# Optimization experiments

Hardware: AMD Instinct MI355X
Metric: run time of the kernel (lower is better)

## Reference

```python
import jax, jax.numpy as jnp
import numpy as np

H, W = 2048, 2048          # frame size (cascade_size)
CS = 227                   # classifier_size
K = 16                     # max components classified per frame (fixed budget)
NC = 4                     # num_classes
THRESH = 0.5               # binarization threshold
MIN_SIZE = 64              # min component pixel count
CC_ITERS = 64              # label-propagation iterations for connected components


def _conv(x, w, stride=1, padding='SAME'):
    return jax.lax.conv_general_dilated(x, w, (stride, stride), padding,
                                        dimension_numbers=('NCHW', 'OIHW', 'NCHW'))


def _cascade(x, w1, w2, w3):
    # stand-in for Unet_plus(1,1): full-res segmentation head -> sigmoid mask
    h = jax.nn.relu(_conv(x, w1))
    h = jax.nn.relu(_conv(h, w2))
    return jax.nn.sigmoid(_conv(h, w3))   # [1,1,H,W]


def _classifier(roi, cw1, cw2, fc):
    # stand-in for CompactNet: roi [B,1,CS,CS] -> logits [B,NC]
    h = jax.nn.relu(_conv(roi, cw1, stride=4, padding='VALID'))
    h = jax.nn.relu(_conv(h, cw2, stride=2, padding='VALID'))
    g = h.mean(axis=(2, 3))               # global average pool -> [B,32]
    return g @ fc


def _connected_components(mask):
    # GPU-style min-index label propagation, 4-connectivity; background label = H*W
    BIG = H * W
    lab = jnp.where(mask, jnp.arange(BIG, dtype=jnp.int32).reshape(H, W), BIG)
    def step(_, lab):
        p = jnp.pad(lab, 1, constant_values=BIG)
        nmin = jnp.minimum(jnp.minimum(p[:-2, 1:-1], p[2:, 1:-1]),
                           jnp.minimum(p[1:-1, :-2], p[1:-1, 2:]))
        return jnp.where(mask, jnp.minimum(lab, nmin), BIG)
    return jax.lax.fori_loop(0, CC_ITERS, step, lab)


def _roi_resize(img, y0, y1, x0, x1):
    # bilinear warp of axis-aligned box [y0:y1, x0:x1] to CS x CS
    t = jnp.linspace(0.0, 1.0, CS)
    gy = y0.astype(jnp.float32) + t * (y1 - y0).astype(jnp.float32)
    gx = x0.astype(jnp.float32) + t * (x1 - x0).astype(jnp.float32)
    yf = jnp.clip(jnp.floor(gy).astype(jnp.int32), 0, H - 2)
    xf = jnp.clip(jnp.floor(gx).astype(jnp.int32), 0, W - 2)
    fy = (gy - yf)[:, None]
    fx = (gx - xf)[None, :]
    v00 = img[yf[:, None], xf[None, :]]
    v01 = img[yf[:, None], (xf + 1)[None, :]]
    v10 = img[(yf + 1)[:, None], xf[None, :]]
    v11 = img[(yf + 1)[:, None], (xf + 1)[None, :]]
    return (1 - fy) * ((1 - fx) * v00 + fx * v01) + fy * ((1 - fx) * v10 + fx * v11)


def _detect(x, w1, w2, w3, cw1, cw2, fc):
    pred_mask = _cascade(x, w1, w2, w3)[0, 0]          # [H,W]
    img = x[0, 0]
    mask = pred_mask > THRESH
    lab = jax.lax.stop_gradient(_connected_components(mask))
    counts = jnp.zeros(H * W + 1, jnp.int32).at[lab.ravel()].add(1)
    counts = counts.at[H * W].set(0)                   # drop background
    cnts, lids = jax.lax.top_k(counts, K)              # K largest components

    def per_comp(lid, cnt):
        cm = lab == lid                                # [H,W] component mask
        valid = (cnt >= MIN_SIZE)
        rowany = cm.any(axis=1)
        colany = cm.any(axis=0)
        y0 = jnp.argmax(rowany); y1 = H - 1 - jnp.argmax(rowany[::-1])
        x0 = jnp.argmax(colany); x1 = W - 1 - jnp.argmax(colany[::-1])
        roi = _roi_resize(img, y0, y1, x0, x1)         # [CS,CS] warped crop
        logits = _classifier(roi[None, None], cw1, cw2, fc)[0]
        return logits, cm, valid

    logits, cms, valids = jax.vmap(per_comp)(lids, cnts)   # [K,NC],[K,H,W],[K]
    return logits, cms, valids


def reference(x, w1, w2, w3, cw1, cw2, fc):
    logits, cms, valids = _detect(x, w1, w2, w3, cw1, cw2, fc)
    onehot = jax.nn.one_hot(jnp.argmax(logits, axis=1), NC) * valids[:, None]
    masks = jnp.einsum('kc,khw->chw', onehot, cms.astype(jnp.float32))
    return jnp.clip(masks, 0.0, 1.0)                   # [NC,H,W] per-class masks


def setup_inputs():
    key = jax.random.key(0)
    ks = jax.random.split(key, 7)
    def nrm(k, shape, fan_in):
        return jax.random.normal(k, shape, jnp.float32) / np.sqrt(fan_in).astype(np.float32)
    return {
        'x':   jax.random.normal(ks[0], (1, 1, H, W), jnp.float32),
        'w1':  nrm(ks[1], (32, 1, 3, 3), 9),
        'w2':  nrm(ks[2], (32, 32, 3, 3), 288),
        'w3':  nrm(ks[3], (1, 32, 1, 1), 32),
        'cw1': nrm(ks[4], (16, 1, 7, 7), 49),
        'cw2': nrm(ks[5], (32, 16, 3, 3), 144),
        'fc':  nrm(ks[6], (32, NC), 32),
    }
```

## Files before the change

### kernel.cpp

```cpp
#include <hip/hip_runtime.h>

#define HH 2048
#define WW 2048
#define HWTOT 4194304
#define BIGL 4194304
#define CSZ 227
#define NCLS 4
#define MINSZ 64
#define TF 1.1920928955078125e-7f
#define EPSB 5e-3f
#define LISTCAP 4000000

#define OFF_LABA 0u
#define OFF_LABB (1u<<24)
#define OFF_H1C  ((1u<<24) + 3538944u)
#define OFF_H2C  ((1u<<24) + 7077888u)
#define OFF_CAND ((1u<<24) + 9437184u)
#define OFF_CAND16 ((1u<<24) + 9437184u + 524288u)
#define OFF_COUNTS (2u<<24)
#define OFF_W2R  ((3u<<24) + 4096u)
#define OFF_W1P  ((3u<<24) + 65536u)
#define OFF_LIST ((3u<<24) + 131072u)

typedef __attribute__((ext_vector_type(8))) short bf16x8;
typedef __attribute__((ext_vector_type(4))) float f32x4;
typedef __attribute__((ext_vector_type(2))) float f32x2;
typedef unsigned int uint;
typedef unsigned short ushort;
typedef unsigned long long u64;

struct Meta {
  int lids[16];
  int valid[16];
  int cls[16];
  int bby0[16], bby1[16], bbx0[16], bbx1[16];
};

__device__ __forceinline__ ushort f2bf(float f) {
  uint u = __float_as_uint(f);
  u += 0x7fffu + ((u >> 16) & 1u);
  return (ushort)(u >> 16);
}
__device__ __forceinline__ float bf2f(ushort h) {
  return __uint_as_float(((uint)h) << 16);
}

#define HSWZ(px, g) ((px) * 32 + ((((g) ^ ((px) & 3) ^ (((px) >> 2) & 3))) << 3))

__global__ __launch_bounds__(256) void prep_kernel(const float* __restrict__ w2,
                                                   const float* __restrict__ w1,
                                                   ushort* __restrict__ wfrag,
                                                   float* __restrict__ w1p) {
  int i = blockIdx.x * 256 + threadIdx.x;
  if (i < 288) {
    int g = i / 72, rem = i - g * 72;
    int t = rem >> 3, r = rem & 7;
    w1p[i] = w1[(g * 8 + r) * 9 + t];
  }
  if (i >= 18432) return;
  int fid = i >> 9, within = i & 511;
  int lane = within >> 3, j = within & 7;
  int tap = fid >> 2, m = (fid >> 1) & 1, p = fid & 1;
  int row = lane & 15, kgrp = lane >> 4;
  int ci = kgrp * 8 + j, oc = m * 16 + row;
  float w = w2[oc * 288 + ci * 9 + tap];
  ushort hb = f2bf(w);
  ushort val = hb;
  if (p) { float lof = w - bf2f(hb); val = f2bf(lof); }
  wfrag[i] = val;
}

__global__ __launch_bounds__(512) void cascade_kernel(
    const float* __restrict__ x, const float* __restrict__ w1p,
    const ushort* __restrict__ wfrag, const float* __restrict__ w3,
    int* __restrict__ lab, int* __restrict__ list, int* __restrict__ list_count) {
  __shared__ float xs[20][36];
  __shared__ __align__(16) short hbuf[2][19584];

  const int tid = threadIdx.x;
  const int ox = blockIdx.x * 32, oy = blockIdx.y * 16;

  for (int i = tid; i < 720; i += 512) {
    int r = i / 36, c = i - r * 36;
    int gy = oy - 2 + r, gx = ox - 2 + c;
    float v = 0.f;
    if ((unsigned)gy < (unsigned)HH && (unsigned)gx < (unsigned)WW) v = x[gy * WW + gx];
    xs[r][c] = v;
  }
  __syncthreads();

  for (int px = tid; px < 612; px += 512) {
    const int hr = px / 34, hc = px - hr * 34;
    const int gy = oy - 1 + hr, gx = ox - 1 + hc;
    const bool inimg = ((unsigned)gy < (unsigned)HH) && ((unsigned)gx < (unsigned)WW);
    float a9[9];
#pragma unroll
    for (int du = 0; du < 3; ++du)
#pragma unroll
      for (int dv = 0; dv < 3; ++dv) a9[du * 3 + dv] = xs[hr + du][hc + dv];
#pragma unroll 1
    for (int g = 0; g < 4; ++g) {
      f32x2 sv2[4];
#pragma unroll
      for (int q = 0; q < 4; ++q) sv2[q] = (f32x2){0.f, 0.f};
#pragma unroll
      for (int t = 0; t < 9; ++t) {
        f32x2 a2 = {a9[t], a9[t]};
        const f32x2* wp = (const f32x2*)&w1p[(g * 9 + t) * 8];
#pragma unroll
        for (int q = 0; q < 4; ++q) {
#if __has_builtin(__builtin_elementwise_fma)
          sv2[q] = __builtin_elementwise_fma(a2, wp[q], sv2[q]);
#else
          sv2[q].x = fmaf(a9[t], wp[q].x, sv2[q].x);
          sv2[q].y = fmaf(a9[t], wp[q].y, sv2[q].y);
#endif
        }
      }
      uint hp[4], lp[4];
#pragma unroll
      for (int q = 0; q < 4; ++q) {
        float s0 = inimg ? fmaxf(sv2[q].x, 0.f) : 0.f;
        float s1 = inimg ? fmaxf(sv2[q].y, 0.f) : 0.f;
        uint h2u;
        asm("v_cvt_pk_bf16_f32 %0, %1, %2" : "=v"(h2u) : "v"(s0), "v"(s1));
        float h0 = __uint_as_float(h2u << 16);
        float h1 = __uint_as_float(h2u & 0xffff0000u);
        uint l2u;
        asm("v_cvt_pk_bf16_f32 %0, %1, %2" : "=v"(l2u) : "v"(s0 - h0), "v"(s1 - h1));
        hp[q] = h2u; lp[q] = l2u;
      }
      *(int4*)&hbuf[0][HSWZ(px, g)] = make_int4(hp[0], hp[1], hp[2], hp[3]);
      *(int4*)&hbuf[1][HSWZ(px, g)] = make_int4(lp[0], lp[1], lp[2], lp[3]);
    }
  }
  __syncthreads();

  const int wv = tid >> 6, lane = tid & 63;
  const int col = lane & 15, kg = lane >> 4;
  const f32x4 zero4 = {0.f, 0.f, 0.f, 0.f};
  f32x4 acc[4][2];
#pragma unroll
  for (int i = 0; i < 4; ++i) { acc[i][0] = zero4; acc[i][1] = zero4; }

  const int4* wf4 = (const int4*)wfrag;
#pragma unroll 3
  for (int tap = 0; tap < 9; ++tap) {
    const int ty = tap / 3, tx = tap - ty * 3;
    bf16x8 a[2][2];
#pragma unroll
    for (int m = 0; m < 2; ++m)
#pragma unroll
      for (int p = 0; p < 2; ++p)
        a[m][p] = __builtin_bit_cast(bf16x8, wf4[(tap * 4 + m * 2 + p) * 64 + lane]);
#pragma unroll
    for (int ni = 0; ni < 4; ++ni) {
      const int nt = wv * 4 + ni;
      const int px = ((nt >> 1) + ty) * 34 + (nt & 1) * 16 + tx + col;
      bf16x8 bh = __builtin_bit_cast(bf16x8, *(const int4*)&hbuf[0][HSWZ(px, kg)]);
      bf16x8 bl = __builtin_bit_cast(bf16x8, *(const int4*)&hbuf[1][HSWZ(px, kg)]);
      acc[ni][0] = __builtin_amdgcn_mfma_f32_16x16x32_bf16(a[0][0], bh, acc[ni][0], 0, 0, 0);
      acc[ni][1] = __builtin_amdgcn_mfma_f32_16x16x32_bf16(a[1][0], bh, acc[ni][1], 0, 0, 0);
      acc[ni][0] = __builtin_amdgcn_mfma_f32_16x16x32_bf16(a[0][1], bh, acc[ni][0], 0, 0, 0);
      acc[ni][1] = __builtin_amdgcn_mfma_f32_16x16x32_bf16(a[1][1], bh, acc[ni][1], 0, 0, 0);
      acc[ni][0] = __builtin_amdgcn_mfma_f32_16x16x32_bf16(a[0][0], bl, acc[ni][0], 0, 0, 0);
      acc[ni][1] = __builtin_amdgcn_mfma_f32_16x16x32_bf16(a[1][0], bl, acc[ni][1], 0, 0, 0);
    }
  }

#pragma unroll 1
  for (int ni = 0; ni < 4; ++ni) {
    const int nt = wv * 4 + ni;
    float z = 0.f;
#pragma unroll
    for (int m = 0; m < 2; ++m)
#pragma unroll
      for (int r = 0; r < 4; ++r)
        z = fmaf(w3[m * 16 + kg * 4 + r], fmaxf(acc[ni][m][r], 0.f), z);
    z += __shfl_xor(z, 16);
    z += __shfl_xor(z, 32);
    const int gy = oy + (nt >> 1), gx = ox + (nt & 1) * 16 + col;
    const int p = gy * WW + gx;
    const bool act = lane < 16;
    if (act) lab[p] = (z > TF) ? p : BIGL;
    bool need = act && (fabsf(z - TF) < EPSB);
    unsigned long long mms = __ballot(need);
    if (mms) {
      int cnt = __popcll(mms);
      int prefix = __popcll(mms & ((1ull << lane) - 1ull));
      int basei = 0;
      if (need && prefix == 0) basei = atomicAdd(list_count, cnt);
      int srcl = __ffsll((long long)mms) - 1;
      basei = __shfl(basei, srcl);
      if (need && basei + prefix < LISTCAP) list[basei + prefix] = p;
    }
  }
}

__global__ __launch_bounds__(256) void recheck_kernel(
    const float* __restrict__ x, const float* __restrict__ w1,
    const float* __restrict__ w2, const float* __restrict__ w3,
    const int* __restrict__ list, const int* __restrict__ list_count,
    int* __restrict__ lab) {
  int n = *list_count;
  if (n > LISTCAP) n = LISTCAP;
  const int half = threadIdx.x & 1;
  for (int i = (blockIdx.x * 256 + threadIdx.x) >> 1; i < n; i += (2048 * 256) >> 1) {
    int p = list[i];
    int py = p >> 11, px = p & 2047;
    float xv[5][5];
#pragma unroll
    for (int u = 0; u < 5; ++u)
#pragma unroll
      for (int v = 0; v < 5; ++v) {
        int gy = py - 2 + u, gx = px - 2 + v;
        xv[u][v] = ((unsigned)gy < (unsigned)HH && (unsigned)gx < (unsigned)WW)
                       ? x[gy * WW + gx] : 0.f;
      }
    double acc2[32];
#pragma unroll
    for (int j = 0; j < 32; ++j) acc2[j] = 0.0;
    const int ci0 = half * 16;
#pragma unroll 1
    for (int ci = ci0; ci < ci0 + 16; ++ci) {
      float h1v[3][3];
#pragma unroll
      for (int u = 0; u < 3; ++u)
#pragma unroll
        for (int v = 0; v < 3; ++v) {
          int gy = py - 1 + u, gx = px - 1 + v;
          float s = 0.f;
#pragma unroll
          for (int t9 = 0; t9 < 9; ++t9)
            s = fmaf(xv[u + t9 / 3][v + t9 % 3], w1[ci * 9 + t9], s);
          bool inb = ((unsigned)gy < (unsigned)HH) && ((unsigned)gx < (unsigned)WW);
          h1v[u][v] = (inb && (s > 0.f)) ? s : 0.f;
        }
#pragma unroll
      for (int dy = 0; dy < 3; ++dy)
#pragma unroll
        for (int dx = 0; dx < 3; ++dx) {
          double hd = (double)h1v[dy][dx];
#pragma unroll
          for (int j = 0; j < 32; ++j)
            acc2[j] = fma(hd, (double)w2[j * 288 + ci * 9 + dy * 3 + dx], acc2[j]);
        }
    }
    double zz = 0.0;
#pragma unroll
    for (int j = 0; j < 32; ++j) {
      double other = __shfl_xor(acc2[j], 1);
      double tot = (half == 0) ? (acc2[j] + other) : (other + acc2[j]);
      zz = fma((double)w3[j], tot > 0.0 ? tot : 0.0, zz);
    }
    if (half == 0) lab[p] = (zz > 1.1920928955078125e-7) ? p : BIGL;
  }
}

__global__ __launch_bounds__(256) void cc16_kernel(const int* __restrict__ in,
                                                   int* __restrict__ out) {
  __shared__ __align__(16) int edgeL[24][100];
  __shared__ __align__(16) int edgeR[24][100];
  __shared__ __align__(16) int4 vtop[8][25];
  __shared__ __align__(16) int4 vbot[8][25];
  const int tid = threadIdx.x;
  const int bx = blockIdx.x & 31, by = blockIdx.x >> 5;
  const int ox0 = bx * 64 - 16, oy0 = by * 64 - 16;
  const bool act = tid < 192;
  const int g = tid % 24, s = tid / 24;
  const int gx = ox0 + g * 4;
  const bool colin = ((unsigned)gx < (unsigned)WW);
  int4 c[12];
#pragma unroll
  for (int r = 0; r < 12; ++r) c[r] = make_int4(BIGL, BIGL, BIGL, BIGL);
  if (act && colin) {
#pragma unroll
    for (int r = 0; r < 12; ++r) {
      int gy = oy0 + s * 12 + r;
      if ((unsigned)gy < (unsigned)HH) c[r] = *(const int4*)(in + gy * WW + gx);
    }
  }
#pragma unroll 1
  for (int step = 0; step < 16; ++step) {
    if (act) {
      *(int4*)&edgeL[g][s * 12 + 0] = make_int4(c[0].x, c[1].x, c[2].x, c[3].x);
      *(int4*)&edgeL[g][s * 12 + 4] = make_int4(c[4].x, c[5].x, c[6].x, c[7].x);
      *(int4*)&edgeL[g][s * 12 + 8] = make_int4(c[8].x, c[9].x, c[10].x, c[11].x);
      *(int4*)&edgeR[g][s * 12 + 0] = make_int4(c[0].w, c[1].w, c[2].w, c[3].w);
      *(int4*)&edgeR[g][s * 12 + 4] = make_int4(c[4].w, c[5].w, c[6].w, c[7].w);
      *(int4*)&edgeR[g][s * 12 + 8] = make_int4(c[8].w, c[9].w, c[10].w, c[11].w);
      vtop[s][g] = c[0];
      vbot[s][g] = c[11];
    }
    __syncthreads();
    if (act) {
      int lf[12], rt[12];
      if (g > 0) {
        int4 a0 = *(const int4*)&edgeR[g - 1][s * 12 + 0];
        int4 a1 = *(const int4*)&edgeR[g - 1][s * 12 + 4];
        int4 a2 = *(const int4*)&edgeR[g - 1][s * 12 + 8];
        lf[0] = a0.x; lf[1] = a0.y; lf[2] = a0.z; lf[3] = a0.w;
        lf[4] = a1.x; lf[5] = a1.y; lf[6] = a1.z; lf[7] = a1.w;
        lf[8] = a2.x; lf[9] = a2.y; lf[10] = a2.z; lf[11] = a2.w;
      } else {
#pragma unroll
        for (int r = 0; r < 12; ++r) lf[r] = BIGL;
      }
      if (g < 23) {
        int4 a0 = *(const int4*)&edgeL[g + 1][s * 12 + 0];
        int4 a1 = *(const int4*)&edgeL[g + 1][s * 12 + 4];
        int4 a2 = *(const int4*)&edgeL[g + 1][s * 12 + 8];
        rt[0] = a0.x; rt[1] = a0.y; rt[2] = a0.z; rt[3] = a0.w;
        rt[4] = a1.x; rt[5] = a1.y; rt[6] = a1.z; rt[7] = a1.w;
        rt[8] = a2.x; rt[9] = a2.y; rt[10] = a2.z; rt[11] = a2.w;
      } else {
#pragma unroll
        for (int r = 0; r < 12; ++r) rt[r] = BIGL;
      }
      int4 prev = (s > 0) ? vbot[s - 1][g] : make_int4(BIGL, BIGL, BIGL, BIGL);
      int4 dnlast = (s < 7) ? vtop[s + 1][g] : make_int4(BIGL, BIGL, BIGL, BIGL);
#pragma unroll
      for (int r = 0; r < 12; ++r) {
        int4 cur = c[r];
        int4 d = (r < 11) ? c[r + 1] : dnlast;
        int4 nr;
        nr.x = (cur.x == BIGL) ? BIGL : min(min(cur.x, cur.y), min(min(prev.x, d.x), lf[r]));
        nr.y = (cur.y == BIGL) ? BIGL : min(min(cur.y, min(cur.x, cur.z)), min(prev.y, d.y));
        nr.z = (cur.z == BIGL) ? BIGL : min(min(cur.z, min(cur.y, cur.w)), min(prev.z, d.z));
        nr.w = (cur.w == BIGL) ? BIGL : min(min(cur.w, min(cur.z, rt[r])), min(prev.w, d.w));
        c[r] = nr;
        prev = cur;
      }
    }
    __syncthreads();
  }
  if (act && g >= 4 && g < 20) {
#pragma unroll
    for (int r = 0; r < 12; ++r) {
      int row = s * 12 + r;
      if (row >= 16 && row < 80) {
        int gy = oy0 + row;
        *(int4*)(out + gy * WW + gx) = c[r];
      }
    }
  }
}

__global__ __launch_bounds__(256) void hist_kernel(const int* __restrict__ lab,
                                                   int* __restrict__ counts) {
  __shared__ int hkey[4096];
  __shared__ int hval[4096];
  int tid = threadIdx.x;
  for (int i = tid; i < 4096; i += 256) { hkey[i] = -1; hval[i] = 0; }
  __syncthreads();
  int t = blockIdx.x * 256 + tid;
  int p = t * 8;
  int4 a = *(const int4*)(lab + p), b = *(const int4*)(lab + p + 4);
  int v[8] = {a.x, a.y, a.z, a.w, b.x, b.y, b.z, b.w};
  int prev = -1, run = 0;
#pragma unroll
  for (int j = 0; j < 8; ++j) {
    int l = v[j];
    if (l == prev) { run++; continue; }
    if (prev >= 0 && prev != BIGL) {
      unsigned hh = (((unsigned)prev * 2654435761u) >> 20) & 4095u;
      for (;;) {
        int k = atomicCAS(&hkey[hh], -1, prev);
        if (k == -1 || k == prev) { atomicAdd(&hval[hh], run); break; }
        hh = (hh + 1) & 4095u;
      }
    }
    prev = l; run = 1;
  }
  if (prev >= 0 && prev != BIGL) {
    unsigned hh = (((unsigned)prev * 2654435761u) >> 20) & 4095u;
    for (;;) {
      int k = atomicCAS(&hkey[hh], -1, prev);
      if (k == -1 || k == prev) { atomicAdd(&hval[hh], run); break; }
      hh = (hh + 1) & 4095u;
    }
  }
  __syncthreads();
  for (int i = tid; i < 4096; i += 256)
    if (hkey[i] >= 0) atomicAdd(&counts[hkey[i]], hval[i]);
}

__global__ __launch_bounds__(256) void cand_kernel(const int* __restrict__ counts,
                                                   int2* __restrict__ cand,
                                                   int* __restrict__ cand_count) {
  int i = blockIdx.x * 256 + threadIdx.x;
  int lane = threadIdx.x & 63;
  int c = (i < HWTOT) ? counts[i] : 0;
  bool hit = (c >= MINSZ);
  unsigned long long m = __ballot(hit);
  if (m) {
    int cnt = __popcll(m);
    int prefix = __popcll(m & ((1ull << lane) - 1ull));
    int base = 0;
    if (hit && prefix == 0) base = atomicAdd(cand_count, cnt);
    int srcl = __ffsll((long long)m) - 1;
    base = __shfl(base, srcl);
    if (hit && base + prefix < 65536) cand[base + prefix] = make_int2(c, i);
  }
}

__global__ __launch_bounds__(256) void top16a_kernel(const int2* __restrict__ cand,
                                                     const int* __restrict__ cand_count,
                                                     u64* __restrict__ cand16) {
  __shared__ u64 skey[256];
  int tid = threadIdx.x;
  int n = *cand_count;
  if (n > 65536) n = 65536;
  u64 prev = ~0ull;
  for (int r = 0; r < 16; ++r) {
    u64 best = 0ull;
    for (int i = blockIdx.x * 256 + tid; i < n; i += 32 * 256) {
      int2 cc = cand[i];
      u64 key = ((u64)(unsigned)cc.x << 32) | (unsigned)(BIGL - cc.y);
      if (key < prev && key > best) best = key;
    }
    skey[tid] = best;
    __syncthreads();
    for (int st = 128; st > 0; st >>= 1) {
      if (tid < st && skey[tid + st] > skey[tid]) skey[tid] = skey[tid + st];
      __syncthreads();
    }
    u64 blockbest = skey[0];
    if (tid == 0) cand16[blockIdx.x * 16 + r] = blockbest;
    prev = blockbest;
    __syncthreads();
  }
}

__global__ __launch_bounds__(256) void top16b_kernel(const u64* __restrict__ cand16,
                                                     Meta* __restrict__ meta) {
  __shared__ u64 skey[256];
  int tid = threadIdx.x;
  u64 k0 = cand16[tid], k1 = cand16[tid + 256];
  u64 prev = ~0ull;
  for (int r = 0; r < 16; ++r) {
    u64 best = 0ull;
    if (k0 < prev && k0 > best) best = k0;
    if (k1 < prev && k1 > best) best = k1;
    skey[tid] = best;
    __syncthreads();
    for (int st = 128; st > 0; st >>= 1) {
      if (tid < st && skey[tid + st] > skey[tid]) skey[tid] = skey[tid + st];
      __syncthreads();
    }
    u64 blockbest = skey[0];
    if (tid == 0) {
      if (blockbest > 0ull) {
        meta->lids[r] = BIGL - (int)(blockbest & 0xffffffffull);
        meta->valid[r] = 1;
      } else {
        meta->lids[r] = -1;
        meta->valid[r] = 0;
      }
    }
    prev = blockbest;
    __syncthreads();
  }
  if (tid < 16) {
    meta->bby0[tid] = HH; meta->bby1[tid] = -1;
    meta->bbx0[tid] = WW; meta->bbx1[tid] = -1;
    meta->cls[tid] = 0;
  }
}

__global__ __launch_bounds__(256) void bbox_kernel(const int* __restrict__ lab,
                                                   Meta* __restrict__ meta) {
  __shared__ int lid_s[16];
  __shared__ int by0[16], by1[16], bx0[16], bx1[16];
  int tid = threadIdx.x;
  if (tid < 16) {
    lid_s[tid] = meta->lids[tid];
    by0[tid] = HH; by1[tid] = -1; bx0[tid] = WW; bx1[tid] = -1;
  }
  __syncthreads();
  int t = blockIdx.x * 256 + tid;
  int p = t * 8;
  int y = p >> 11, xbase = p & 2047;
  int4 a = *(const int4*)(lab + p), b = *(const int4*)(lab + p + 4);
  int v[8] = {a.x, a.y, a.z, a.w, b.x, b.y, b.z, b.w};
  int prev = BIGL, kprev = -1, xs = 0, xe = 0;
#pragma unroll
  for (int j = 0; j < 8; ++j) {
    int l = v[j];
    if (l == prev) { xe = xbase + j; continue; }
    if (kprev >= 0) {
      atomicMin(&by0[kprev], y); atomicMax(&by1[kprev], y);
      atomicMin(&bx0[kprev], xs); atomicMax(&bx1[kprev], xe);
    }
    prev = l; xs = xe = xbase + j; kprev = -1;
    if (l != BIGL) {
      for (int k = 0; k < 16; ++k)
        if (lid_s[k] == l) { kprev = k; break; }
    }
  }
  if (kprev >= 0) {
    atomicMin(&by0[kprev], y); atomicMax(&by1[kprev], y);
    atomicMin(&bx0[kprev], xs); atomicMax(&bx1[kprev], xe);
  }
  __syncthreads();
  if (tid < 16 && by1[tid] >= 0) {
    atomicMin(&meta->bby0[tid], by0[tid]); atomicMax(&meta->bby1[tid], by1[tid]);
    atomicMin(&meta->bbx0[tid], bx0[tid]); atomicMax(&meta->bbx1[tid], bx1[tid]);
  }
}

__global__ __launch_bounds__(256) void cconv1_kernel(const float* __restrict__ img,
                                                     const float* __restrict__ cw1,
                                                     const Meta* __restrict__ meta,
                                                     float* __restrict__ h1c) {
  int k = blockIdx.y, oy = blockIdx.x;
  if (!meta->valid[k]) return;
  __shared__ float srow[7][CSZ];
  float y0 = (float)meta->bby0[k], y1 = (float)meta->bby1[k];
  float x0 = (float)meta->bbx0[k], x1 = (float)meta->bbx1[k];
  for (int idx = threadIdx.x; idx < 7 * CSZ; idx += 256) {
    int rr = idx / CSZ, j = idx - rr * CSZ;
    int i = oy * 4 + rr;
    float ti = (float)i / 226.f, tj = (float)j / 226.f;
    float gy = y0 + ti * (y1 - y0);
    float gx = x0 + tj * (x1 - x0);
    int yf = (int)floorf(gy); yf = yf < 0 ? 0 : (yf > HH - 2 ? HH - 2 : yf);
    int xf = (int)floorf(gx); xf = xf < 0 ? 0 : (xf > WW - 2 ? WW - 2 : xf);
    float fy = gy - (float)yf, fx = gx - (float)xf;
    const float* r0 = img + yf * WW + xf;
    float v00 = r0[0], v01 = r0[1], v10 = r0[WW], v11 = r0[WW + 1];
    srow[rr][j] = (1.f - fy) * ((1.f - fx) * v00 + fx * v01) +
                  fy * ((1.f - fx) * v10 + fx * v11);
  }
  __syncthreads();
  for (int idx = threadIdx.x; idx < 16 * 56; idx += 256) {
    int ch = idx / 56, ox = idx - ch * 56;
    const float* wp = cw1 + ch * 49;
    float s = 0.f;
#pragma unroll
    for (int dy = 0; dy < 7; ++dy)
#pragma unroll
      for (int dx = 0; dx < 7; ++dx)
        s += srow[dy][ox * 4 + dx] * wp[dy * 7 + dx];
    h1c[((k * 16 + ch) * 56 + oy) * 56 + ox] = s > 0.f ? s : 0.f;
  }
}

__global__ __launch_bounds__(256) void cconv2_kernel(const float* __restrict__ h1c,
                                                     const float* __restrict__ cw2,
                                                     const Meta* __restrict__ meta,
                                                     float* __restrict__ h2c) {
  int k = blockIdx.y, oy = blockIdx.x;
  if (!meta->valid[k]) return;
  for (int idx = threadIdx.x; idx < 32 * 27; idx += 256) {
    int ch = idx / 27, ox = idx - ch * 27;
    float s = 0.f;
    for (int ci = 0; ci < 16; ++ci) {
      const float* hp = h1c + ((k * 16 + ci) * 56 + oy * 2) * 56 + ox * 2;
      const float* wp = cw2 + (ch * 16 + ci) * 9;
#pragma unroll
      for (int dy = 0; dy < 3; ++dy)
#pragma unroll
        for (int dx = 0; dx < 3; ++dx) s += hp[dy * 56 + dx] * wp[dy * 3 + dx];
    }
    h2c[((k * 32 + ch) * 27 + oy) * 27 + ox] = s > 0.f ? s : 0.f;
  }
}

__global__ __launch_bounds__(256) void poolfc_kernel(const float* __restrict__ h2c,
                                                     const float* __restrict__ fc,
                                                     Meta* __restrict__ meta) {
  int k = blockIdx.x;
  if (!meta->valid[k]) return;
  __shared__ float sums[8][32];
  int tid = threadIdx.x;
  int c = tid & 31, part = tid >> 5;
  float s = 0.f;
  const float* hp = h2c + (k * 32 + c) * 729;
  for (int j = part; j < 729; j += 8) s += hp[j];
  sums[part][c] = s;
  __syncthreads();
  if (tid < 32) {
    float g = 0.f;
#pragma unroll
    for (int p2 = 0; p2 < 8; ++p2) g += sums[p2][tid];
    sums[0][tid] = g / 729.f;
  }
  __syncthreads();
  if (tid == 0) {
    float best = -1e30f;
    int bi = 0;
    for (int j = 0; j < NCLS; ++j) {
      float lg = 0.f;
      for (int c2 = 0; c2 < 32; ++c2) lg += sums[0][c2] * fc[c2 * NCLS + j];
      if (lg > best) { best = lg; bi = j; }
    }
    meta->cls[k] = bi;
  }
}

__global__ __launch_bounds__(256) void final_kernel(const float* labf,
                                                    const Meta* __restrict__ meta,
                                                    float* out) {
  __shared__ int lid_s[16];
  __shared__ int cls_s[16];
  int tid = threadIdx.x;
  if (tid < 16) {
    lid_s[tid] = meta->valid[tid] ? meta->lids[tid] : -1;
    cls_s[tid] = meta->cls[tid];
  }
  __syncthreads();
  int t = blockIdx.x * 256 + tid;
  int p = t * 4;
  float4 lf = *(const float4*)(labf + p);
  int l4[4] = {__float_as_int(lf.x), __float_as_int(lf.y), __float_as_int(lf.z),
               __float_as_int(lf.w)};
  int cj[4];
#pragma unroll
  for (int j = 0; j < 4; ++j) {
    cj[j] = -1;
    int l = l4[j];
    if (l != BIGL) {
      for (int k = 0; k < 16; ++k)
        if (lid_s[k] == l) { cj[j] = cls_s[k]; break; }
    }
  }
#pragma unroll
  for (int c = 0; c < 4; ++c) {
    float4 w4 = make_float4(cj[0] == c ? 1.f : 0.f, cj[1] == c ? 1.f : 0.f,
                            cj[2] == c ? 1.f : 0.f, cj[3] == c ? 1.f : 0.f);
    *(float4*)(out + (size_t)c * HWTOT + p) = w4;
  }
}

extern "C" void kernel_launch(void* const* d_in, const int* in_sizes, int n_in,
                              void* d_out, int out_size, void* d_ws, size_t ws_size,
                              hipStream_t stream) {
  const float* x = (const float*)d_in[0];
  const float* w1 = (const float*)d_in[1];
  const float* w2 = (const float*)d_in[2];
  const float* w3 = (const float*)d_in[3];
  const float* cw1 = (const float*)d_in[4];
  const float* cw2 = (const float*)d_in[5];
  const float* fc = (const float*)d_in[6];

  char* base = (char*)d_out;
  int* lab_a = (int*)(base + OFF_LABA);
  int* lab_b = (int*)(base + OFF_LABB);
  float* h1c = (float*)(base + OFF_H1C);
  float* h2c = (float*)(base + OFF_H2C);
  int2* cand = (int2*)(base + OFF_CAND);
  u64* cand16 = (u64*)(base + OFF_CAND16);
  int* counts = (int*)(base + OFF_COUNTS);
  ushort* wfrag = (ushort*)(base + OFF_W2R);
  float* w1p = (float*)(base + OFF_W1P);
  int* list = (int*)(base + OFF_LIST);
  int* cand_count = (int*)d_ws;
  int* list_count = (int*)((char*)d_ws + 64);
  Meta* meta = (Meta*)((char*)d_ws + 256);

  hipMemsetAsync(counts, 0, (size_t)(HWTOT + 1) * sizeof(int), stream);
  hipMemsetAsync(d_ws, 0, 128, stream);

  prep_kernel<<<72, 256, 0, stream>>>(w2, w1, wfrag, w1p);
  cascade_kernel<<<dim3(64, 128), 512, 0, stream>>>(x, w1p, wfrag, w3, lab_a, list,
                                                    list_count);
  recheck_kernel<<<2048, 256, 0, stream>>>(x, w1, w2, w3, list, list_count, lab_a);

  for (int l = 0; l < 4; ++l) {
    const int* src = (l & 1) ? lab_b : lab_a;
    int* dst = (l & 1) ? lab_a : lab_b;
    cc16_kernel<<<1024, 256, 0, stream>>>(src, dst);
  }

  hist_kernel<<<2048, 256, 0, stream>>>(lab_a, counts);
  cand_kernel<<<16384, 256, 0, stream>>>(counts, cand, cand_count);
  top16a_kernel<<<32, 256, 0, stream>>>(cand, cand_count, cand16);
  top16b_kernel<<<1, 256, 0, stream>>>(cand16, meta);
  bbox_kernel<<<2048, 256, 0, stream>>>(lab_a, meta);
  cconv1_kernel<<<dim3(56, 16), 256, 0, stream>>>(x, cw1, meta, h1c);
  cconv2_kernel<<<dim3(27, 16), 256, 0, stream>>>(h1c, cw2, meta, h2c);
  poolfc_kernel<<<16, 256, 0, stream>>>(h2c, fc, meta);
  final_kernel<<<4096, 256, 0, stream>>>((const float*)d_out, meta, (float*)d_out);
}
```

Baseline: 661.1 us.

## Fuse label histogram into last CC pass, add early exit, drop workspace memset

```diff
diff --git a/kernel.cpp b/kernel.cpp
--- a/kernel.cpp
+++ b/kernel.cpp
@@ -36,6 +36,13 @@
   int bby0[16], bby1[16], bbx0[16], bbx1[16];
 };
 
+struct CCShared {
+  int edgeL[24][100];
+  int edgeR[24][100];
+  int4 vtop[8][25];
+  int4 vbot[8][25];
+};
+
 __device__ __forceinline__ ushort f2bf(float f) {
   uint u = __float_as_uint(f);
   u += 0x7fffu + ((u >> 16) & 1u);
@@ -50,7 +57,9 @@
 __global__ __launch_bounds__(256) void prep_kernel(const float* __restrict__ w2,
                                                    const float* __restrict__ w1,
                                                    ushort* __restrict__ wfrag,
-                                                   float* __restrict__ w1p) {
+                                                   float* __restrict__ w1p,
+                                                   int* __restrict__ ws) {
+  if (blockIdx.x == 0 && threadIdx.x < 32) ws[threadIdx.x] = 0;
   int i = blockIdx.x * 256 + threadIdx.x;
   if (i < 288) {
     int g = i / 72, rem = i - g * 72;
@@ -257,12 +266,22 @@
   }
 }
 
+__device__ __forceinline__ void hist_add(int* hkey, int* hval, int label, int run) {
+  unsigned hh = (((unsigned)label * 2654435761u) >> 20) & 4095u;
+  for (;;) {
+    int k = atomicCAS(&hkey[hh], -1, label);
+    if (k == -1 || k == label) { atomicAdd(&hval[hh], run); break; }
+    hh = (hh + 1) & 4095u;
+  }
+}
+
 __global__ __launch_bounds__(256) void cc16_kernel(const int* __restrict__ in,
-                                                   int* __restrict__ out) {
-  __shared__ __align__(16) int edgeL[24][100];
-  __shared__ __align__(16) int edgeR[24][100];
-  __shared__ __align__(16) int4 vtop[8][25];
-  __shared__ __align__(16) int4 vbot[8][25];
+                                                   int* __restrict__ out,
+                                                   int* __restrict__ counts,
+                                                   int dohist) {
+  __shared__ __align__(16) char smem[32768];
+  CCShared* S = (CCShared*)smem;
+  __shared__ int chg[2];
   const int tid = threadIdx.x;
   const int bx = blockIdx.x & 31, by = blockIdx.x >> 5;
   const int ox0 = bx * 64 - 16, oy0 = by * 64 - 16;
@@ -280,25 +299,31 @@
       if ((unsigned)gy < (unsigned)HH) c[r] = *(const int4*)(in + gy * WW + gx);
     }
   }
+  if (tid < 2) chg[tid] = 1;
+  __syncthreads();
+
 #pragma unroll 1
   for (int step = 0; step < 16; ++step) {
+    const int cur = step & 1, nxt = cur ^ 1;
     if (act) {
-      *(int4*)&edgeL[g][s * 12 + 0] = make_int4(c[0].x, c[1].x, c[2].x, c[3].x);
-      *(int4*)&edgeL[g][s * 12 + 4] = make_int4(c[4].x, c[5].x, c[6].x, c[7].x);
-      *(int4*)&edgeL[g][s * 12 + 8] = make_int4(c[8].x, c[9].x, c[10].x, c[11].x);
-      *(int4*)&edgeR[g][s * 12 + 0] = make_int4(c[0].w, c[1].w, c[2].w, c[3].w);
-      *(int4*)&edgeR[g][s * 12 + 4] = make_int4(c[4].w, c[5].w, c[6].w, c[7].w);
-      *(int4*)&edgeR[g][s * 12 + 8] = make_int4(c[8].w, c[9].w, c[10].w, c[11].w);
-      vtop[s][g] = c[0];
-      vbot[s][g] = c[11];
-    }
-    __syncthreads();
+      *(int4*)&S->edgeL[g][s * 12 + 0] = make_int4(c[0].x, c[1].x, c[2].x, c[3].x);
+      *(int4*)&S->edgeL[g][s * 12 + 4] = make_int4(c[4].x, c[5].x, c[6].x, c[7].x);
+      *(int4*)&S->edgeL[g][s * 12 + 8] = make_int4(c[8].x, c[9].x, c[10].x, c[11].x);
+      *(int4*)&S->edgeR[g][s * 12 + 0] = make_int4(c[0].w, c[1].w, c[2].w, c[3].w);
+      *(int4*)&S->edgeR[g][s * 12 + 4] = make_int4(c[4].w, c[5].w, c[6].w, c[7].w);
+      *(int4*)&S->edgeR[g][s * 12 + 8] = make_int4(c[8].w, c[9].w, c[10].w, c[11].w);
+      S->vtop[s][g] = c[0];
+      S->vbot[s][g] = c[11];
+    }
+    if (tid == 0) chg[nxt] = 0;
+    __syncthreads();
+    if (chg[cur] == 0) break;
     if (act) {
       int lf[12], rt[12];
       if (g > 0) {
-        int4 a0 = *(const int4*)&edgeR[g - 1][s * 12 + 0];
-        int4 a1 = *(const int4*)&edgeR[g - 1][s * 12 + 4];
-        int4 a2 = *(const int4*)&edgeR[g - 1][s * 12 + 8];
+        int4 a0 = *(const int4*)&S->edgeR[g - 1][s * 12 + 0];
+        int4 a1 = *(const int4*)&S->edgeR[g - 1][s * 12 + 4];
+        int4 a2 = *(const int4*)&S->edgeR[g - 1][s * 12 + 8];
         lf[0] = a0.x; lf[1] = a0.y; lf[2] = a0.z; lf[3] = a0.w;
         lf[4] = a1.x; lf[5] = a1.y; lf[6] = a1.z; lf[7] = a1.w;
         lf[8] = a2.x; lf[9] = a2.y; lf[10] = a2.z; lf[11] = a2.w;
@@ -307,9 +332,9 @@
         for (int r = 0; r < 12; ++r) lf[r] = BIGL;
       }
       if (g < 23) {
-        int4 a0 = *(const int4*)&edgeL[g + 1][s * 12 + 0];
-        int4 a1 = *(const int4*)&edgeL[g + 1][s * 12 + 4];
-        int4 a2 = *(const int4*)&edgeL[g + 1][s * 12 + 8];
+        int4 a0 = *(const int4*)&S->edgeL[g + 1][s * 12 + 0];
+        int4 a1 = *(const int4*)&S->edgeL[g + 1][s * 12 + 4];
+        int4 a2 = *(const int4*)&S->edgeL[g + 1][s * 12 + 8];
         rt[0] = a0.x; rt[1] = a0.y; rt[2] = a0.z; rt[3] = a0.w;
         rt[4] = a1.x; rt[5] = a1.y; rt[6] = a1.z; rt[7] = a1.w;
         rt[8] = a2.x; rt[9] = a2.y; rt[10] = a2.z; rt[11] = a2.w;
@@ -317,23 +342,55 @@
 #pragma unroll
         for (int r = 0; r < 12; ++r) rt[r] = BIGL;
       }
-      int4 prev = (s > 0) ? vbot[s - 1][g] : make_int4(BIGL, BIGL, BIGL, BIGL);
-      int4 dnlast = (s < 7) ? vtop[s + 1][g] : make_int4(BIGL, BIGL, BIGL, BIGL);
+      int4 prev = (s > 0) ? S->vbot[s - 1][g] : make_int4(BIGL, BIGL, BIGL, BIGL);
+      int4 dnlast = (s < 7) ? S->vtop[s + 1][g] : make_int4(BIGL, BIGL, BIGL, BIGL);
+      int diff = 0;
 #pragma unroll
       for (int r = 0; r < 12; ++r) {
-        int4 cur = c[r];
+        int4 cc2 = c[r];
         int4 d = (r < 11) ? c[r + 1] : dnlast;
         int4 nr;
-        nr.x = (cur.x == BIGL) ? BIGL : min(min(cur.x, cur.y), min(min(prev.x, d.x), lf[r]));
-        nr.y = (cur.y == BIGL) ? BIGL : min(min(cur.y, min(cur.x, cur.z)), min(prev.y, d.y));
-        nr.z = (cur.z == BIGL) ? BIGL : min(min(cur.z, min(cur.y, cur.w)), min(prev.z, d.z));
-        nr.w = (cur.w == BIGL) ? BIGL : min(min(cur.w, min(cur.z, rt[r])), min(prev.w, d.w));
+        nr.x = (cc2.x == BIGL) ? BIGL : min(min(cc2.x, cc2.y), min(min(prev.x, d.x), lf[r]));
+        nr.y = (cc2.y == BIGL) ? BIGL : min(min(cc2.y, min(cc2.x, cc2.z)), min(prev.y, d.y));
+        nr.z = (cc2.z == BIGL) ? BIGL : min(min(cc2.z, min(cc2.y, cc2.w)), min(prev.z, d.z));
+        nr.w = (cc2.w == BIGL) ? BIGL : min(min(cc2.w, min(cc2.z, rt[r])), min(prev.w, d.w));
+        diff |= (nr.x != cc2.x) | (nr.y != cc2.y) | (nr.z != cc2.z) | (nr.w != cc2.w);
         c[r] = nr;
-        prev = cur;
-      }
-    }
-    __syncthreads();
-  }
+        prev = cc2;
+      }
+      if (diff) chg[nxt] = 1;
+    }
+    __syncthreads();
+  }
+
+  if (dohist) {
+    int* hkey = (int*)smem;
+    int* hval = (int*)(smem + 16384);
+    __syncthreads();
+    for (int i = tid; i < 4096; i += 256) { hkey[i] = -1; hval[i] = 0; }
+    __syncthreads();
+    if (act && g >= 4 && g < 20) {
+      int prevl = -1, run = 0;
+#pragma unroll 1
+      for (int r = 0; r < 12; ++r) {
+        int row = s * 12 + r;
+        if (row < 16 || row >= 80) continue;
+        int v[4] = {c[r].x, c[r].y, c[r].z, c[r].w};
+#pragma unroll
+        for (int j = 0; j < 4; ++j) {
+          int l = v[j];
+          if (l == prevl) { run++; continue; }
+          if (prevl >= 0 && prevl != BIGL) hist_add(hkey, hval, prevl, run);
+          prevl = l; run = 1;
+        }
+      }
+      if (prevl >= 0 && prevl != BIGL) hist_add(hkey, hval, prevl, run);
+    }
+    __syncthreads();
+    for (int i = tid; i < 4096; i += 256)
+      if (hkey[i] >= 0) atomicAdd(&counts[hkey[i]], hval[i]);
+  }
+
   if (act && g >= 4 && g < 20) {
 #pragma unroll
     for (int r = 0; r < 12; ++r) {
@@ -344,45 +401,6 @@
       }
     }
   }
-}
-
-__global__ __launch_bounds__(256) void hist_kernel(const int* __restrict__ lab,
-                                                   int* __restrict__ counts) {
-  __shared__ int hkey[4096];
-  __shared__ int hval[4096];
-  int tid = threadIdx.x;
-  for (int i = tid; i < 4096; i += 256) { hkey[i] = -1; hval[i] = 0; }
-  __syncthreads();
-  int t = blockIdx.x * 256 + tid;
-  int p = t * 8;
-  int4 a = *(const int4*)(lab + p), b = *(const int4*)(lab + p + 4);
-  int v[8] = {a.x, a.y, a.z, a.w, b.x, b.y, b.z, b.w};
-  int prev = -1, run = 0;
-#pragma unroll
-  for (int j = 0; j < 8; ++j) {
-    int l = v[j];
-    if (l == prev) { run++; continue; }
-    if (prev >= 0 && prev != BIGL) {
-      unsigned hh = (((unsigned)prev * 2654435761u) >> 20) & 4095u;
-      for (;;) {
-        int k = atomicCAS(&hkey[hh], -1, prev);
-        if (k == -1 || k == prev) { atomicAdd(&hval[hh], run); break; }
-        hh = (hh + 1) & 4095u;
-      }
-    }
-    prev = l; run = 1;
-  }
-  if (prev >= 0 && prev != BIGL) {
-    unsigned hh = (((unsigned)prev * 2654435761u) >> 20) & 4095u;
-    for (;;) {
-      int k = atomicCAS(&hkey[hh], -1, prev);
-      if (k == -1 || k == prev) { atomicAdd(&hval[hh], run); break; }
-      hh = (hh + 1) & 4095u;
-    }
-  }
-  __syncthreads();
-  for (int i = tid; i < 4096; i += 256)
-    if (hkey[i] >= 0) atomicAdd(&counts[hkey[i]], hval[i]);
 }
 
 __global__ __launch_bounds__(256) void cand_kernel(const int* __restrict__ counts,
@@ -660,20 +678,17 @@
   Meta* meta = (Meta*)((char*)d_ws + 256);
 
   hipMemsetAsync(counts, 0, (size_t)(HWTOT + 1) * sizeof(int), stream);
-  hipMemsetAsync(d_ws, 0, 128, stream);
-
-  prep_kernel<<<72, 256, 0, stream>>>(w2, w1, wfrag, w1p);
+
+  prep_kernel<<<72, 256, 0, stream>>>(w2, w1, wfrag, w1p, (int*)d_ws);
   cascade_kernel<<<dim3(64, 128), 512, 0, stream>>>(x, w1p, wfrag, w3, lab_a, list,
                                                     list_count);
   recheck_kernel<<<2048, 256, 0, stream>>>(x, w1, w2, w3, list, list_count, lab_a);
 
-  for (int l = 0; l < 4; ++l) {
-    const int* src = (l & 1) ? lab_b : lab_a;
-    int* dst = (l & 1) ? lab_a : lab_b;
-    cc16_kernel<<<1024, 256, 0, stream>>>(src, dst);
-  }
-
-  hist_kernel<<<2048, 256, 0, stream>>>(lab_a, counts);
+  cc16_kernel<<<1024, 256, 0, stream>>>(lab_a, lab_b, counts, 0);
+  cc16_kernel<<<1024, 256, 0, stream>>>(lab_b, lab_a, counts, 0);
+  cc16_kernel<<<1024, 256, 0, stream>>>(lab_a, lab_b, counts, 0);
+  cc16_kernel<<<1024, 256, 0, stream>>>(lab_b, lab_a, counts, 1);
+
   cand_kernel<<<16384, 256, 0, stream>>>(counts, cand, cand_count);
   top16a_kernel<<<32, 256, 0, stream>>>(cand, cand_count, cand16);
   top16b_kernel<<<1, 256, 0, stream>>>(cand16, meta);
```

After: 749.5 us. 13.4% more time.
